# Performance work log

Measured on AMD Instinct MI355X. Metric: run time of the kernel, lower is better.

Reference implementation:

```python
import jax, jax.numpy as jnp
import numpy as np

B, T, I, H = 2048, 4096, 5, 10  # batch, seq_len, input_dim, hidden_dim


def setup_inputs() -> dict:
    key = jax.random.key(0)
    ks = jax.random.split(key, 5)
    return {
        "x": jax.random.normal(ks[0], (B, T, I), dtype=jnp.float32),
        "h0": jnp.zeros((1, B, H), dtype=jnp.float32),
        "c0": jnp.zeros((1, B, H), dtype=jnp.float32),
        "W_ih": jax.random.normal(ks[1], (4 * H, I), dtype=jnp.float32) * 0.3,
        "W_hh": jax.random.normal(ks[2], (4 * H, H), dtype=jnp.float32) * 0.3,
        "b_ih": jax.random.normal(ks[3], (4 * H,), dtype=jnp.float32) * 0.1,
        "b_hh": jax.random.normal(ks[4], (4 * H,), dtype=jnp.float32) * 0.1,
    }


def reference(x, h0, c0, W_ih, W_hh, b_ih, b_hh):
    # Single-layer nn.LSTM (batch_first=True), gate order i,f,g,o.
    # Precompute input contribution for all timesteps: [B,T,4H]
    x_gates = jnp.einsum("bti,gi->btg", x, W_ih) + b_ih + b_hh

    def step(carry, xg_t):
        h, c = carry  # [B,H] each
        gates = xg_t + h @ W_hh.T  # [B,4H]
        i_g, f_g, g_g, o_g = jnp.split(gates, 4, axis=-1)
        i_g = jax.nn.sigmoid(i_g)
        f_g = jax.nn.sigmoid(f_g)
        g_g = jnp.tanh(g_g)
        o_g = jax.nn.sigmoid(o_g)
        c = f_g * c + i_g * g_g
        h = o_g * jnp.tanh(c)
        return (h, c), h

    (_, _), hs = jax.lax.scan(step, (h0[0], c0[0]), jnp.swapaxes(x_gates, 0, 1))
    return jnp.swapaxes(hs, 0, 1)  # [B,T,H], matching lstm_out
```

## Files before the change

### kernel.cpp

```cpp
#include <hip/hip_runtime.h>


#define BB 2048
#define TT 4096
#define II 5
#define HH 10
#define CH 256
#define CHF (CH * II)
#define NCHUNK (TT / CH)

__device__ __forceinline__ float readlane_f(float v, int l) {
    union { float f; int i; } u;
    u.f = v;
    u.i = __builtin_amdgcn_readlane(u.i, l);
    return u.f;
}

template<int E>
__device__ __forceinline__ float quad_bcast(float v) {
    union { float f; int i; } u;
    u.f = v;
    u.i = __builtin_amdgcn_update_dpp(u.i, u.i, E * 0x55, 0xF, 0xF, false);
    return u.f;
}

__global__ __launch_bounds__(64) void lstm_wave_kernel(
    const float* __restrict__ x,
    const float* __restrict__ h0,
    const float* __restrict__ c0,
    const float* __restrict__ W_ih,
    const float* __restrict__ W_hh,
    const float* __restrict__ b_ih,
    const float* __restrict__ b_hh,
    float* __restrict__ out)
{
    __shared__ float xs[2][CHF];

    const int b = blockIdx.x;
    const int lane = threadIdx.x;
    const int j = lane >> 2;
    const int k = lane & 3;
    const bool active = (lane < 4 * HH);

    const float LOG2E = 1.4426950408889634f;
    const float KC = -2.f * LOG2E;
    const float scale = (k == 2) ? KC : -LOG2E;

    float wih[II];
    float whh[HH];
    float bias = 0.f;
    if (active) {
        const int row = k * HH + j;
#pragma unroll
        for (int q = 0; q < II; q++) wih[q] = W_ih[row * II + q] * scale;
#pragma unroll
        for (int q = 0; q < HH; q++) whh[q] = W_hh[row * HH + q] * scale;
        bias = (b_ih[row] + b_hh[row]) * scale;
    } else {
#pragma unroll
        for (int q = 0; q < II; q++) wih[q] = 0.f;
#pragma unroll
        for (int q = 0; q < HH; q++) whh[q] = 0.f;
    }

    const float am = (k == 2) ? (2.f * KC) : 1.f;
    const float ac = (k == 2) ? (-KC) : 0.f;

    float hval = 0.f, cs = 0.f;
    if (active) {
        hval = h0[b * HH + j];
        cs   = c0[b * HH + j] * KC;
    }

    const float* xrow = x + (size_t)b * TT * II;
    float* orow = out + (size_t)b * TT * HH;
    const bool do_store = active && (k == 0);

    float4 pf0, pf1, pf2, pf3, pf4;
    {
        const float4* xv = (const float4*)xrow;
        pf0 = xv[0 * 64 + lane];
        pf1 = xv[1 * 64 + lane];
        pf2 = xv[2 * 64 + lane];
        pf3 = xv[3 * 64 + lane];
        pf4 = xv[4 * 64 + lane];
        float4* dst = (float4*)xs[0];
        dst[0 * 64 + lane] = pf0;
        dst[1 * 64 + lane] = pf1;
        dst[2 * 64 + lane] = pf2;
        dst[3 * 64 + lane] = pf3;
        dst[4 * 64 + lane] = pf4;
    }

    for (int c = 0; c < NCHUNK; ++c) {
        const float* xc = xs[c & 1];

        if (c + 1 < NCHUNK) {
            const float4* xv = (const float4*)(xrow + (size_t)(c + 1) * CHF);
            pf0 = xv[0 * 64 + lane];
            pf1 = xv[1 * 64 + lane];
            pf2 = xv[2 * 64 + lane];
            pf3 = xv[3 * 64 + lane];
            pf4 = xv[4 * 64 + lane];
        }

#pragma unroll 8
        for (int u = 0; u < CH; ++u) {
            const int t = c * CH + u;

            const float x0 = xc[u * II + 0];
            const float x1 = xc[u * II + 1];
            const float x2 = xc[u * II + 2];
            const float x3 = xc[u * II + 3];
            const float x4 = xc[u * II + 4];

            float a0 = fmaf(x0, wih[0], bias);
            float a1 = x1 * wih[1];
            float a2 = x2 * wih[2];
            float a3 = x3 * wih[3];
            a0 = fmaf(x4, wih[4], a0);

            a0 = fmaf(readlane_f(hval, 0),  whh[0], a0);
            a1 = fmaf(readlane_f(hval, 4),  whh[1], a1);
            a2 = fmaf(readlane_f(hval, 8),  whh[2], a2);
            a3 = fmaf(readlane_f(hval, 12), whh[3], a3);
            a0 = fmaf(readlane_f(hval, 16), whh[4], a0);
            a1 = fmaf(readlane_f(hval, 20), whh[5], a1);
            a2 = fmaf(readlane_f(hval, 24), whh[6], a2);
            a3 = fmaf(readlane_f(hval, 28), whh[7], a3);
            a0 = fmaf(readlane_f(hval, 32), whh[8], a0);
            a1 = fmaf(readlane_f(hval, 36), whh[9], a1);
            const float acc = (a0 + a1) + (a2 + a3);

            const float e = __builtin_amdgcn_exp2f(acc);
            const float s = __builtin_amdgcn_rcpf(1.f + e);
            const float act = fmaf(s, am, ac);

            const float iv = quad_bcast<0>(act);
            const float fv = quad_bcast<1>(act);
            const float gs = quad_bcast<2>(act);
            const float ov = quad_bcast<3>(act);

            cs = fmaf(fv, cs, iv * gs);
            const float e2 = __builtin_amdgcn_exp2f(cs);
            const float th = fmaf(__builtin_amdgcn_rcpf(1.f + e2), 2.f, -1.f);
            hval = ov * th;

            if (do_store) orow[t * HH + j] = hval;
        }

        if (c + 1 < NCHUNK) {
            float4* dst = (float4*)xs[(c + 1) & 1];
            dst[0 * 64 + lane] = pf0;
            dst[1 * 64 + lane] = pf1;
            dst[2 * 64 + lane] = pf2;
            dst[3 * 64 + lane] = pf3;
            dst[4 * 64 + lane] = pf4;
        }
    }
}

extern "C" void kernel_launch(void* const* d_in, const int* in_sizes, int n_in,
                              void* d_out, int out_size, void* d_ws, size_t ws_size,
                              hipStream_t stream) {
    const float* x    = (const float*)d_in[0];
    const float* h0   = (const float*)d_in[1];
    const float* c0   = (const float*)d_in[2];
    const float* W_ih = (const float*)d_in[3];
    const float* W_hh = (const float*)d_in[4];
    const float* b_ih = (const float*)d_in[5];
    const float* b_hh = (const float*)d_in[6];
    float* out = (float*)d_out;

    lstm_wave_kernel<<<dim3(BB), dim3(64), 0, stream>>>(
        x, h0, c0, W_ih, W_hh, b_ih, b_hh, out);
}
```

Measured before the change: 1.117 ms.

## Pad LDS x rows for vector reads and batch output stores across lanes

```diff
diff --git a/kernel.cpp b/kernel.cpp
--- a/kernel.cpp
+++ b/kernel.cpp
@@ -7,6 +7,8 @@
 #define HH 10
 #define CH 256
 #define CHF (CH * II)
+#define PSTRIDE 32
+#define BUFB (CH * PSTRIDE)
 #define NCHUNK (TT / CH)
 
 __device__ __forceinline__ float readlane_f(float v, int l) {
@@ -34,7 +36,7 @@
     const float* __restrict__ b_hh,
     float* __restrict__ out)
 {
-    __shared__ float xs[2][CHF];
+    __shared__ __align__(16) char xs[2][BUFB];
 
     const int b = blockIdx.x;
     const int lane = threadIdx.x;
@@ -73,52 +75,55 @@
     }
 
     const float* xrow = x + (size_t)b * TT * II;
-    float* orow = out + (size_t)b * TT * HH;
-    const bool do_store = active && (k == 0);
 
-    float4 pf0, pf1, pf2, pf3, pf4;
+    float* outp = out + (size_t)b * TT * HH + k * HH + j;
+
+    int wa[II][4];
+#pragma unroll
+    for (int q = 0; q < II; q++) {
+#pragma unroll
+        for (int c4 = 0; c4 < 4; c4++) {
+            const int p = (q * 64 + lane) * 4 + c4;
+            wa[q][c4] = (p / II) * PSTRIDE + (p % II) * 4;
+        }
+    }
+
+    float4 pf[II];
     {
         const float4* xv = (const float4*)xrow;
-        pf0 = xv[0 * 64 + lane];
-        pf1 = xv[1 * 64 + lane];
-        pf2 = xv[2 * 64 + lane];
-        pf3 = xv[3 * 64 + lane];
-        pf4 = xv[4 * 64 + lane];
-        float4* dst = (float4*)xs[0];
-        dst[0 * 64 + lane] = pf0;
-        dst[1 * 64 + lane] = pf1;
-        dst[2 * 64 + lane] = pf2;
-        dst[3 * 64 + lane] = pf3;
-        dst[4 * 64 + lane] = pf4;
+#pragma unroll
+        for (int q = 0; q < II; q++) pf[q] = xv[q * 64 + lane];
+        char* dst = xs[0];
+#pragma unroll
+        for (int q = 0; q < II; q++) {
+            *(float*)(dst + wa[q][0]) = pf[q].x;
+            *(float*)(dst + wa[q][1]) = pf[q].y;
+            *(float*)(dst + wa[q][2]) = pf[q].z;
+            *(float*)(dst + wa[q][3]) = pf[q].w;
+        }
     }
 
+    float keep = 0.f;
+
     for (int c = 0; c < NCHUNK; ++c) {
-        const float* xc = xs[c & 1];
+        const char* xc = xs[c & 1];
 
         if (c + 1 < NCHUNK) {
             const float4* xv = (const float4*)(xrow + (size_t)(c + 1) * CHF);
-            pf0 = xv[0 * 64 + lane];
-            pf1 = xv[1 * 64 + lane];
-            pf2 = xv[2 * 64 + lane];
-            pf3 = xv[3 * 64 + lane];
-            pf4 = xv[4 * 64 + lane];
+#pragma unroll
+            for (int q = 0; q < II; q++) pf[q] = xv[q * 64 + lane];
         }
 
 #pragma unroll 8
         for (int u = 0; u < CH; ++u) {
-            const int t = c * CH + u;
+            const float4 xv4 = *(const float4*)(xc + u * PSTRIDE);
+            const float x4v  = *(const float*)(xc + u * PSTRIDE + 16);
 
-            const float x0 = xc[u * II + 0];
-            const float x1 = xc[u * II + 1];
-            const float x2 = xc[u * II + 2];
-            const float x3 = xc[u * II + 3];
-            const float x4 = xc[u * II + 4];
-
-            float a0 = fmaf(x0, wih[0], bias);
-            float a1 = x1 * wih[1];
-            float a2 = x2 * wih[2];
-            float a3 = x3 * wih[3];
-            a0 = fmaf(x4, wih[4], a0);
+            float a0 = fmaf(xv4.x, wih[0], bias);
+            float a1 = xv4.y * wih[1];
+            float a2 = xv4.z * wih[2];
+            float a3 = xv4.w * wih[3];
+            a0 = fmaf(x4v, wih[4], a0);
 
             a0 = fmaf(readlane_f(hval, 0),  whh[0], a0);
             a1 = fmaf(readlane_f(hval, 4),  whh[1], a1);
@@ -146,16 +151,23 @@
             const float th = fmaf(__builtin_amdgcn_rcpf(1.f + e2), 2.f, -1.f);
             hval = ov * th;
 
-            if (do_store) orow[t * HH + j] = hval;
+            keep = ((u & 3) == k) ? hval : keep;
+            if ((u & 3) == 3) {
+                const int off = ((u & 7) == 3) ? 0 : 40;
+                if (active) outp[off] = keep;
+            }
+            if ((u & 7) == 7) outp += 80;
         }
 
         if (c + 1 < NCHUNK) {
-            float4* dst = (float4*)xs[(c + 1) & 1];
-            dst[0 * 64 + lane] = pf0;
-            dst[1 * 64 + lane] = pf1;
-            dst[2 * 64 + lane] = pf2;
-            dst[3 * 64 + lane] = pf3;
-            dst[4 * 64 + lane] = pf4;
+            char* dst = xs[(c + 1) & 1];
+#pragma unroll
+            for (int q = 0; q < II; q++) {
+                *(float*)(dst + wa[q][0]) = pf[q].x;
+                *(float*)(dst + wa[q][1]) = pf[q].y;
+                *(float*)(dst + wa[q][2]) = pf[q].z;
+                *(float*)(dst + wa[q][3]) = pf[q].w;
+            }
         }
     }
 }
```

Result: faster. 1.059 ms (-5.3%).
